# Kernel optimization log

Hardware: AMD Instinct MI355X
Metric: run time of the kernel (lower is better)

## Reference

```python
import jax, jax.numpy as jnp
import numpy as np

N_NODES = 100000
N_EDGES = 1600000
S_FEAT = 16   # static node features
D_FEAT = 8    # dynamic node features
E_FEAT = 4    # edge features
K = 2
EDGE_IN = E_FEAT + 2 * S_FEAT + 2 * D_FEAT  # 52
HIDDEN = 2 * D_FEAT                          # 16


def setup_inputs() -> dict:
    key = jax.random.key(0)
    ks = jax.random.split(key, 12)
    inp = {
        "x_s": jax.random.normal(ks[0], (N_NODES, S_FEAT), jnp.float32),
        "x_d": jax.random.normal(ks[1], (N_NODES, D_FEAT), jnp.float32),
        "edge_attr": jax.random.normal(ks[2], (N_EDGES, E_FEAT), jnp.float32),
        # edge MLP: Linear(EDGE_IN->HIDDEN) + ReLU + Linear(HIDDEN->D_FEAT)
        "W1": jax.random.normal(ks[3], (HIDDEN, EDGE_IN), jnp.float32) / np.sqrt(EDGE_IN),
        "b1": jnp.zeros((HIDDEN,), jnp.float32),
        "W2": jax.random.normal(ks[4], (D_FEAT, HIDDEN), jnp.float32) / np.sqrt(HIDDEN),
        "b2": jnp.zeros((D_FEAT,), jnp.float32),
        # K+1 = 3 filter matrices, Linear(D->D, bias=False): y = x @ W.T
        "Wf0": jax.random.normal(ks[5], (D_FEAT, D_FEAT), jnp.float32) / np.sqrt(D_FEAT),
        "Wf1": jax.random.normal(ks[6], (D_FEAT, D_FEAT), jnp.float32) / np.sqrt(D_FEAT),
        "Wf2": jax.random.normal(ks[7], (D_FEAT, D_FEAT), jnp.float32) / np.sqrt(D_FEAT),
        "edge_index": jax.random.randint(ks[8], (2, N_EDGES), 0, N_NODES, jnp.int64
                                         if jax.config.jax_enable_x64 else jnp.int32),
    }
    return inp


def _edge_mlp(e, W1, b1, W2, b2):
    h = jax.nn.relu(e @ W1.T + b1)
    return h @ W2.T + b2


def reference(x_s, x_d, edge_attr, W1, b1, W2, b2, Wf0, Wf1, Wf2, edge_index):
    row, col = edge_index[0], edge_index[1]
    num_nodes = x_d.shape[0]

    # s_ij depends only on static inputs (x_s, x_d, edge_attr), not on `out`,
    # so it is identical across the K steps; compute it once. The per-step
    # boolean edge mask is applied multiplicatively below, which matches the
    # torch masked-gather/scatter exactly (normalization is per-edge).
    e_ij = jnp.concatenate(
        [x_s[row], x_s[col], x_d[row], x_d[col], edge_attr], axis=1)  # [E, 52]
    s_ij = _edge_mlp(e_ij, W1, b1, W2, b2)                            # [E, D]
    nrm = jnp.linalg.norm(s_ij, axis=1, keepdims=True)
    s_ij = jnp.where(nrm > 0, s_ij / jnp.where(nrm > 0, nrm, 1.0), 0.0)

    filters = [Wf0, Wf1, Wf2]
    out = x_d @ filters[0].T
    for k in range(K):
        mask = out.sum(1) != 0                         # [N]
        edge_mask = (mask[row] | mask[col]).astype(out.dtype)  # [E]
        hydraulic_gradient = out[col] - out[row]       # [E, D]
        shift_sum = hydraulic_gradient * s_ij * edge_mask[:, None]
        scattered = jax.ops.segment_sum(shift_sum, col, num_segments=num_nodes)
        scattered = scattered @ filters[k + 1].T
        out = out + scattered
    return out
```

## Files before the change

kernel.cpp:

```cpp
#include <hip/hip_runtime.h>

#define S_FEAT 16
#define D_FEAT 8
#define E_FEAT 4
#define EDGE_IN 52
#define HIDDEN 16
#define SCAN_CHUNK 2048
#define NSUB 8

typedef unsigned int uint4v __attribute__((ext_vector_type(4)));

__device__ __forceinline__ void mlp_sij(
    const float* __restrict__ x_s, const float* __restrict__ x_d,
    const float* __restrict__ edge_attr,
    const float* __restrict__ W1, const float* __restrict__ b1,
    const float* __restrict__ W2, const float* __restrict__ b2,
    int row, int col, int e, float s[D_FEAT])
{
    float in[EDGE_IN];
    {
        const float4* p = (const float4*)(x_s + (size_t)row * S_FEAT);
#pragma unroll
        for (int q = 0; q < 4; ++q) {
            float4 v = p[q];
            in[q * 4 + 0] = v.x; in[q * 4 + 1] = v.y;
            in[q * 4 + 2] = v.z; in[q * 4 + 3] = v.w;
        }
    }
    {
        const float4* p = (const float4*)(x_s + (size_t)col * S_FEAT);
#pragma unroll
        for (int q = 0; q < 4; ++q) {
            float4 v = p[q];
            in[16 + q * 4 + 0] = v.x; in[16 + q * 4 + 1] = v.y;
            in[16 + q * 4 + 2] = v.z; in[16 + q * 4 + 3] = v.w;
        }
    }
    {
        const float4* p = (const float4*)(x_d + (size_t)row * D_FEAT);
#pragma unroll
        for (int q = 0; q < 2; ++q) {
            float4 v = p[q];
            in[32 + q * 4 + 0] = v.x; in[32 + q * 4 + 1] = v.y;
            in[32 + q * 4 + 2] = v.z; in[32 + q * 4 + 3] = v.w;
        }
    }
    {
        const float4* p = (const float4*)(x_d + (size_t)col * D_FEAT);
#pragma unroll
        for (int q = 0; q < 2; ++q) {
            float4 v = p[q];
            in[40 + q * 4 + 0] = v.x; in[40 + q * 4 + 1] = v.y;
            in[40 + q * 4 + 2] = v.z; in[40 + q * 4 + 3] = v.w;
        }
    }
    {
        float4 v = *(const float4*)(edge_attr + (size_t)e * E_FEAT);
        in[48] = v.x; in[49] = v.y; in[50] = v.z; in[51] = v.w;
    }

    float h[HIDDEN];
#pragma unroll
    for (int i = 0; i < HIDDEN; ++i) {
        float acc = b1[i];
#pragma unroll
        for (int j = 0; j < EDGE_IN; ++j)
            acc = fmaf(in[j], W1[i * EDGE_IN + j], acc);
        h[i] = acc > 0.f ? acc : 0.f;
    }

    float nrm2 = 0.f;
#pragma unroll
    for (int i = 0; i < D_FEAT; ++i) {
        float acc = b2[i];
#pragma unroll
        for (int j = 0; j < HIDDEN; ++j)
            acc = fmaf(h[j], W2[i * HIDDEN + j], acc);
        s[i] = acc;
        nrm2 = fmaf(acc, acc, nrm2);
    }
    float nrm = sqrtf(nrm2);
    float inv = nrm > 0.f ? 1.f / nrm : 0.f;
#pragma unroll
    for (int i = 0; i < D_FEAT; ++i) s[i] *= inv;
}

__device__ __forceinline__ uint4v pack_rec(const float s[8], int row)
{
    int q[8];
#pragma unroll
    for (int i = 0; i < 8; ++i) {
        float v = fminf(fmaxf(s[i] * 2047.f, -2047.f), 2047.f);
        q[i] = (int)rintf(v) & 0xFFF;
    }
    uint4v r;
    r[0] = (unsigned)(q[0] | (q[1] << 12) | (q[2] << 24));
    r[1] = (unsigned)((q[2] >> 8) | (q[3] << 4) | (q[4] << 16) | (q[5] << 28));
    r[2] = (unsigned)((q[5] >> 4) | (q[6] << 8) | (q[7] << 20));
    r[3] = (unsigned)row;
    return r;
}

__device__ __forceinline__ float rec_s(uint4v r, int f)
{
    int off = f * 12;
    unsigned lo = off < 32 ? r[0] : (off < 64 ? r[1] : r[2]);
    unsigned hi = off < 32 ? r[1] : (off < 64 ? r[2] : 0u);
    unsigned sh = (unsigned)off & 31u;
    unsigned long long both = ((unsigned long long)hi << 32) | lo;
    int q = ((int)((unsigned)(both >> sh) << 20)) >> 20;
    return (float)q * (1.f / 2047.f);
}

__global__ __launch_bounds__(256) void zero_counts_kernel(int* __restrict__ counts, int M)
{
    int i = blockIdx.x * blockDim.x + threadIdx.x;
    if (i < M) counts[i] = 0;
}

__global__ __launch_bounds__(256) void hist_kernel(
    const int* __restrict__ ei, int E, int N, int* __restrict__ counts8)
{
    int e = blockIdx.x * blockDim.x + threadIdx.x;
    if (e >= E) return;
    int col = ei[E + e];
    atomicAdd(&counts8[(threadIdx.x & (NSUB - 1)) * N + col], 1);
}

__global__ __launch_bounds__(256) void scan_local_kernel(
    const int* __restrict__ counts8, int* __restrict__ partial,
    int* __restrict__ blocksums, int N)
{
    __shared__ int sh[256];
    int b = blockIdx.x, t = threadIdx.x;
    int base = b * SCAN_CHUNK + t * 8;
    int v[8];
    int run = 0;
#pragma unroll
    for (int j = 0; j < 8; ++j) {
        int c = 0;
        if (base + j < N) {
#pragma unroll
            for (int s8 = 0; s8 < NSUB; ++s8)
                c += counts8[s8 * N + base + j];
        }
        v[j] = run;
        run += c;
    }
    sh[t] = run;
    __syncthreads();
#pragma unroll
    for (int st = 1; st < 256; st <<= 1) {
        int x = (t >= st) ? sh[t - st] : 0;
        __syncthreads();
        sh[t] += x;
        __syncthreads();
    }
    int excl = sh[t] - run;
    if (t == 255) blocksums[b] = sh[255];
#pragma unroll
    for (int j = 0; j < 8; ++j)
        if (base + j < N) partial[base + j] = excl + v[j];
}

__global__ void scan_blk_kernel(int* __restrict__ blocksums, int NB)
{
    if (threadIdx.x == 0) {
        int run = 0;
        for (int i = 0; i < NB; ++i) { int c = blocksums[i]; blocksums[i] = run; run += c; }
    }
}

__global__ __launch_bounds__(256) void scan_add_kernel(
    int* __restrict__ offsets, int* __restrict__ cursor,
    const int* __restrict__ blocksums, int N, int E)
{
    int i = blockIdx.x * blockDim.x + threadIdx.x;
    if (i < N) {
        int off = offsets[i] + blocksums[i / SCAN_CHUNK];
        offsets[i] = off;
        cursor[i]  = off;
    } else if (i == N) {
        offsets[N] = E;
    }
}

__global__ __launch_bounds__(256) void mlp_scatter_kernel(
    const float* __restrict__ x_s, const float* __restrict__ x_d,
    const float* __restrict__ edge_attr,
    const float* __restrict__ W1, const float* __restrict__ b1,
    const float* __restrict__ W2, const float* __restrict__ b2,
    const int* __restrict__ ei, int E,
    int* __restrict__ cursor, uint4v* __restrict__ recs)
{
    int e = blockIdx.x * blockDim.x + threadIdx.x;
    if (e >= E) return;
    int row = ei[e], col = ei[E + e];
    float s[D_FEAT];
    mlp_sij(x_s, x_d, edge_attr, W1, b1, W2, b2, row, col, e, s);
    uint4v rec = pack_rec(s, row);
    int pos = atomicAdd(&cursor[col], 1);
    __builtin_nontemporal_store(rec, recs + pos);
}

__global__ __launch_bounds__(256) void node_init_kernel(
    const float* __restrict__ x_d, const float* __restrict__ Wf0,
    float* __restrict__ out, unsigned char* __restrict__ mask, int N)
{
    int n = blockIdx.x * blockDim.x + threadIdx.x;
    if (n >= N) return;
    float xd[D_FEAT];
    {
        const float4* p = (const float4*)(x_d + (size_t)n * D_FEAT);
        float4 a = p[0], b = p[1];
        xd[0] = a.x; xd[1] = a.y; xd[2] = a.z; xd[3] = a.w;
        xd[4] = b.x; xd[5] = b.y; xd[6] = b.z; xd[7] = b.w;
    }
    float o[D_FEAT];
    float rs = 0.f;
#pragma unroll
    for (int i = 0; i < D_FEAT; ++i) {
        float acc = 0.f;
#pragma unroll
        for (int j = 0; j < D_FEAT; ++j)
            acc = fmaf(xd[j], Wf0[i * D_FEAT + j], acc);
        o[i] = acc;
        rs += acc;
    }
    float4* op = (float4*)(out + (size_t)n * D_FEAT);
    op[0] = make_float4(o[0], o[1], o[2], o[3]);
    op[1] = make_float4(o[4], o[5], o[6], o[7]);
    mask[n] = (rs != 0.f) ? 1 : 0;
}

__global__ __launch_bounds__(256) void csr_step_kernel(
    const float* __restrict__ out_in, float* __restrict__ out_out,
    const unsigned char* __restrict__ mask_in, unsigned char* __restrict__ mask_out,
    const int* __restrict__ offsets, const uint4v* __restrict__ recs,
    const float* __restrict__ Wf, int N)
{
    int lane = threadIdx.x & 63;
    int node = blockIdx.x * 4 + (threadIdx.x >> 6);
    if (node >= N) return;
    int e_sub = lane >> 3, f = lane & 7;
    int beg = offsets[node], end = offsets[node + 1];
    float outc = out_in[(size_t)node * 8 + f];
    int mc = mask_in[node];
    float acc = 0.f;
    for (int base = beg; base < end; base += 8) {
        int e = base + e_sub;
        bool valid = e < end;
        uint4v rec = (uint4v)(0u);
        if (valid) rec = __builtin_nontemporal_load(recs + e);
        int row = (int)rec[3];
        float s = rec_s(rec, f);
        float outr = out_in[(size_t)row * 8 + f];
        int m = mc | (int)mask_in[row];
        acc += (m != 0) ? (outc - outr) * s : 0.f;
    }
    acc += __shfl_xor(acc, 8);
    acc += __shfl_xor(acc, 16);
    acc += __shfl_xor(acc, 32);
    float upd = 0.f;
#pragma unroll
    for (int j = 0; j < 8; ++j) {
        float aj = __shfl(acc, (lane & ~7) | j);
        upd = fmaf(Wf[f * 8 + j], aj, upd);
    }
    float o = outc + upd;
    float rs = o;
    rs += __shfl_xor(rs, 1);
    rs += __shfl_xor(rs, 2);
    rs += __shfl_xor(rs, 4);
    if (e_sub == 0) {
        out_out[(size_t)node * 8 + f] = o;
        if (f == 0) mask_out[node] = (rs != 0.f) ? 1 : 0;
    }
}

__global__ __launch_bounds__(256) void fb_node_init_kernel(
    const float* __restrict__ x_d, const float* __restrict__ Wf0,
    float* __restrict__ out, float* __restrict__ scattered, int N)
{
    int n = blockIdx.x * blockDim.x + threadIdx.x;
    if (n >= N) return;
    float xd[D_FEAT];
    const float4* p = (const float4*)(x_d + (size_t)n * D_FEAT);
    float4 a = p[0], b = p[1];
    xd[0] = a.x; xd[1] = a.y; xd[2] = a.z; xd[3] = a.w;
    xd[4] = b.x; xd[5] = b.y; xd[6] = b.z; xd[7] = b.w;
    float o[D_FEAT];
#pragma unroll
    for (int i = 0; i < D_FEAT; ++i) {
        float acc = 0.f;
#pragma unroll
        for (int j = 0; j < D_FEAT; ++j)
            acc = fmaf(xd[j], Wf0[i * D_FEAT + j], acc);
        o[i] = acc;
    }
    float4* op = (float4*)(out + (size_t)n * D_FEAT);
    op[0] = make_float4(o[0], o[1], o[2], o[3]);
    op[1] = make_float4(o[4], o[5], o[6], o[7]);
    float4* sp = (float4*)(scattered + (size_t)n * D_FEAT);
    sp[0] = make_float4(0.f, 0.f, 0.f, 0.f);
    sp[1] = make_float4(0.f, 0.f, 0.f, 0.f);
}

__global__ __launch_bounds__(256) void fb_edge_step_kernel(
    const float* __restrict__ x_s, const float* __restrict__ x_d,
    const float* __restrict__ edge_attr,
    const float* __restrict__ W1, const float* __restrict__ b1,
    const float* __restrict__ W2, const float* __restrict__ b2,
    const float* __restrict__ out,
    const int* __restrict__ ei, int E, float* __restrict__ scattered)
{
    int e = blockIdx.x * blockDim.x + threadIdx.x;
    if (e >= E) return;
    int row = ei[e], col = ei[E + e];
    const float4* pr = (const float4*)(out + (size_t)row * D_FEAT);
    const float4* pc = (const float4*)(out + (size_t)col * D_FEAT);
    float4 r0 = pr[0], r1 = pr[1], c0 = pc[0], c1 = pc[1];
    float srow = r0.x + r0.y + r0.z + r0.w + r1.x + r1.y + r1.z + r1.w;
    float scol = c0.x + c0.y + c0.z + c0.w + c1.x + c1.y + c1.z + c1.w;
    if (srow == 0.f && scol == 0.f) return;
    float s[D_FEAT];
    mlp_sij(x_s, x_d, edge_attr, W1, b1, W2, b2, row, col, e, s);
    float* dst = scattered + (size_t)col * D_FEAT;
    atomicAdd(dst + 0, (c0.x - r0.x) * s[0]);
    atomicAdd(dst + 1, (c0.y - r0.y) * s[1]);
    atomicAdd(dst + 2, (c0.z - r0.z) * s[2]);
    atomicAdd(dst + 3, (c0.w - r0.w) * s[3]);
    atomicAdd(dst + 4, (c1.x - r1.x) * s[4]);
    atomicAdd(dst + 5, (c1.y - r1.y) * s[5]);
    atomicAdd(dst + 6, (c1.z - r1.z) * s[6]);
    atomicAdd(dst + 7, (c1.w - r1.w) * s[7]);
}

__global__ __launch_bounds__(256) void fb_node_update_kernel(
    float* __restrict__ out, float* __restrict__ scattered,
    const float* __restrict__ Wf, int N)
{
    int n = blockIdx.x * blockDim.x + threadIdx.x;
    if (n >= N) return;
    float sc[D_FEAT];
    float4* sp = (float4*)(scattered + (size_t)n * D_FEAT);
    float4 a = sp[0], b = sp[1];
    sc[0] = a.x; sc[1] = a.y; sc[2] = a.z; sc[3] = a.w;
    sc[4] = b.x; sc[5] = b.y; sc[6] = b.z; sc[7] = b.w;
    sp[0] = make_float4(0.f, 0.f, 0.f, 0.f);
    sp[1] = make_float4(0.f, 0.f, 0.f, 0.f);
    float4* op = (float4*)(out + (size_t)n * D_FEAT);
    float4 o0 = op[0], o1 = op[1];
    float o[D_FEAT] = {o0.x, o0.y, o0.z, o0.w, o1.x, o1.y, o1.z, o1.w};
#pragma unroll
    for (int i = 0; i < D_FEAT; ++i) {
        float acc = 0.f;
#pragma unroll
        for (int j = 0; j < D_FEAT; ++j)
            acc = fmaf(sc[j], Wf[i * D_FEAT + j], acc);
        o[i] += acc;
    }
    op[0] = make_float4(o[0], o[1], o[2], o[3]);
    op[1] = make_float4(o[4], o[5], o[6], o[7]);
}

extern "C" void kernel_launch(void* const* d_in, const int* in_sizes, int n_in,
                              void* d_out, int out_size, void* d_ws, size_t ws_size,
                              hipStream_t stream) {
    const float* x_s       = (const float*)d_in[0];
    const float* x_d       = (const float*)d_in[1];
    const float* edge_attr = (const float*)d_in[2];
    const float* W1        = (const float*)d_in[3];
    const float* b1        = (const float*)d_in[4];
    const float* W2        = (const float*)d_in[5];
    const float* b2        = (const float*)d_in[6];
    const float* Wf[3]     = {(const float*)d_in[7], (const float*)d_in[8],
                              (const float*)d_in[9]};
    const int*   ei        = (const int*)d_in[10];

    const int N = in_sizes[1] / D_FEAT;
    const int E = in_sizes[10] / 2;

    float* out = (float*)d_out;

    size_t off = 0;
    auto carve = [&](size_t bytes) { size_t p = off; off = (off + bytes + 255) & ~255ULL; return p; };
    size_t o_counts  = carve((size_t)NSUB * N * 4);
    size_t o_offsets = carve((size_t)(N + 1) * 4);
    size_t o_cursor  = carve((size_t)(N + 1) * 4);
    size_t o_bsums   = carve(256 * 4);
    size_t o_maskA   = carve((size_t)N);
    size_t o_maskB   = carve((size_t)N);
    size_t o_bufA    = carve((size_t)N * D_FEAT * 4);
    size_t o_recs    = carve((size_t)E * 16);
    const size_t need = off;

    dim3 blk(256);
    dim3 gE((E + 255) / 256);
    dim3 gN((N + 255) / 256);

    if (ws_size >= need) {
        char* ws = (char*)d_ws;
        int*   counts8 = (int*)(ws + o_counts);
        int*   offsets = (int*)(ws + o_offsets);
        int*   cursor  = (int*)(ws + o_cursor);
        int*   bsums   = (int*)(ws + o_bsums);
        unsigned char* maskA = (unsigned char*)(ws + o_maskA);
        unsigned char* maskB = (unsigned char*)(ws + o_maskB);
        float* bufA    = (float*)(ws + o_bufA);
        uint4v* recs   = (uint4v*)(ws + o_recs);

        const int NB = (N + SCAN_CHUNK - 1) / SCAN_CHUNK;

        zero_counts_kernel<<<dim3((NSUB * N + 255) / 256), blk, 0, stream>>>(counts8, NSUB * N);
        hist_kernel<<<gE, blk, 0, stream>>>(ei, E, N, counts8);
        scan_local_kernel<<<dim3(NB), blk, 0, stream>>>(counts8, offsets, bsums, N);
        scan_blk_kernel<<<dim3(1), dim3(64), 0, stream>>>(bsums, NB);
        scan_add_kernel<<<dim3((N + 256) / 256), blk, 0, stream>>>(offsets, cursor, bsums, N, E);

        node_init_kernel<<<gN, blk, 0, stream>>>(x_d, Wf[0], out, maskA, N);
        mlp_scatter_kernel<<<gE, blk, 0, stream>>>(
            x_s, x_d, edge_attr, W1, b1, W2, b2, ei, E, cursor, recs);

        dim3 gC((N + 3) / 4);
        csr_step_kernel<<<gC, blk, 0, stream>>>(
            out, bufA, maskA, maskB, offsets, recs, Wf[1], N);
        csr_step_kernel<<<gC, blk, 0, stream>>>(
            bufA, out, maskB, maskA, offsets, recs, Wf[2], N);
    } else {
        float* scattered = (float*)d_ws;
        fb_node_init_kernel<<<gN, blk, 0, stream>>>(x_d, Wf[0], out, scattered, N);
        for (int k = 0; k < 2; ++k) {
            fb_edge_step_kernel<<<gE, blk, 0, stream>>>(
                x_s, x_d, edge_attr, W1, b1, W2, b2, out, ei, E, scattered);
            fb_node_update_kernel<<<gN, blk, 0, stream>>>(out, scattered, Wf[k + 1], N);
        }
    }
}
```

Baseline: 419.7 us.

## Precompute per-node first-layer projections and derive masks from out in-register

Splits the first edge-MLP layer by linearity into per-node projections (row part with bias, col part) computed once per node. The edge kernel then gathers two 16-float vectors plus edge_attr instead of 48 input floats, and does only the 4-wide edge-feature part of the matmul. The per-node mask byte arrays are also removed: the CSR step recomputes each node's nonzero-sum mask from the gathered out row with lane shuffles. This trades extra workspace (two N×16 buffers) and one more launch, plus extra shuffles in the gather loop, for fewer FLOPs and a smaller per-edge gather.

```diff
diff --git a/kernel.cpp b/kernel.cpp
--- a/kernel.cpp
+++ b/kernel.cpp
@@ -185,7 +185,114 @@
     }
 }
 
-__global__ __launch_bounds__(256) void mlp_scatter_kernel(
+__global__ __launch_bounds__(256) void proj_kernel(
+    const float* __restrict__ x_s, const float* __restrict__ x_d,
+    const float* __restrict__ W1, const float* __restrict__ b1,
+    float* __restrict__ PR, float* __restrict__ PC, int N)
+{
+    int n = blockIdx.x * blockDim.x + threadIdx.x;
+    if (n >= N) return;
+    float xs[S_FEAT], xd[D_FEAT];
+    {
+        const float4* p = (const float4*)(x_s + (size_t)n * S_FEAT);
+#pragma unroll
+        for (int q = 0; q < 4; ++q) {
+            float4 v = p[q];
+            xs[q * 4 + 0] = v.x; xs[q * 4 + 1] = v.y;
+            xs[q * 4 + 2] = v.z; xs[q * 4 + 3] = v.w;
+        }
+        const float4* pd = (const float4*)(x_d + (size_t)n * D_FEAT);
+        float4 a = pd[0], b = pd[1];
+        xd[0] = a.x; xd[1] = a.y; xd[2] = a.z; xd[3] = a.w;
+        xd[4] = b.x; xd[5] = b.y; xd[6] = b.z; xd[7] = b.w;
+    }
+    float pr[HIDDEN], pc[HIDDEN];
+#pragma unroll
+    for (int i = 0; i < HIDDEN; ++i) {
+        const float* w = W1 + i * EDGE_IN;
+        float a = b1[i], c = 0.f;
+#pragma unroll
+        for (int j = 0; j < S_FEAT; ++j) {
+            a = fmaf(xs[j], w[j], a);
+            c = fmaf(xs[j], w[16 + j], c);
+        }
+#pragma unroll
+        for (int j = 0; j < D_FEAT; ++j) {
+            a = fmaf(xd[j], w[32 + j], a);
+            c = fmaf(xd[j], w[40 + j], c);
+        }
+        pr[i] = a; pc[i] = c;
+    }
+    float4* prp = (float4*)(PR + (size_t)n * HIDDEN);
+    float4* pcp = (float4*)(PC + (size_t)n * HIDDEN);
+#pragma unroll
+    for (int q = 0; q < 4; ++q) {
+        prp[q] = make_float4(pr[q * 4], pr[q * 4 + 1], pr[q * 4 + 2], pr[q * 4 + 3]);
+        pcp[q] = make_float4(pc[q * 4], pc[q * 4 + 1], pc[q * 4 + 2], pc[q * 4 + 3]);
+    }
+}
+
+__global__ __launch_bounds__(256) void mlp_scatter_proj_kernel(
+    const float* __restrict__ PR, const float* __restrict__ PC,
+    const float* __restrict__ edge_attr,
+    const float* __restrict__ W1,
+    const float* __restrict__ W2, const float* __restrict__ b2,
+    const int* __restrict__ ei, int E,
+    int* __restrict__ cursor, uint4v* __restrict__ recs)
+{
+    int e = blockIdx.x * blockDim.x + threadIdx.x;
+    if (e >= E) return;
+    int row = ei[e], col = ei[E + e];
+
+    float pr[HIDDEN], pc[HIDDEN];
+    {
+        const float4* p = (const float4*)(PR + (size_t)row * HIDDEN);
+        const float4* c = (const float4*)(PC + (size_t)col * HIDDEN);
+#pragma unroll
+        for (int q = 0; q < 4; ++q) {
+            float4 a = p[q], b = c[q];
+            pr[q * 4 + 0] = a.x; pr[q * 4 + 1] = a.y;
+            pr[q * 4 + 2] = a.z; pr[q * 4 + 3] = a.w;
+            pc[q * 4 + 0] = b.x; pc[q * 4 + 1] = b.y;
+            pc[q * 4 + 2] = b.z; pc[q * 4 + 3] = b.w;
+        }
+    }
+    float4 ea = *(const float4*)(edge_attr + (size_t)e * E_FEAT);
+
+    float h[HIDDEN];
+#pragma unroll
+    for (int i = 0; i < HIDDEN; ++i) {
+        const float* w = W1 + i * EDGE_IN + 48;
+        float acc = pr[i] + pc[i];
+        acc = fmaf(ea.x, w[0], acc);
+        acc = fmaf(ea.y, w[1], acc);
+        acc = fmaf(ea.z, w[2], acc);
+        acc = fmaf(ea.w, w[3], acc);
+        h[i] = acc > 0.f ? acc : 0.f;
+    }
+
+    float s[D_FEAT];
+    float nrm2 = 0.f;
+#pragma unroll
+    for (int i = 0; i < D_FEAT; ++i) {
+        float acc = b2[i];
+#pragma unroll
+        for (int j = 0; j < HIDDEN; ++j)
+            acc = fmaf(h[j], W2[i * HIDDEN + j], acc);
+        s[i] = acc;
+        nrm2 = fmaf(acc, acc, nrm2);
+    }
+    float nrm = sqrtf(nrm2);
+    float inv = nrm > 0.f ? 1.f / nrm : 0.f;
+#pragma unroll
+    for (int i = 0; i < D_FEAT; ++i) s[i] *= inv;
+
+    uint4v rec = pack_rec(s, row);
+    int pos = atomicAdd(&cursor[col], 1);
+    __builtin_nontemporal_store(rec, recs + pos);
+}
+
+__global__ __launch_bounds__(256) void mlp_scatter_direct_kernel(
     const float* __restrict__ x_s, const float* __restrict__ x_d,
     const float* __restrict__ edge_attr,
     const float* __restrict__ W1, const float* __restrict__ b1,
@@ -205,7 +312,7 @@
 
 __global__ __launch_bounds__(256) void node_init_kernel(
     const float* __restrict__ x_d, const float* __restrict__ Wf0,
-    float* __restrict__ out, unsigned char* __restrict__ mask, int N)
+    float* __restrict__ out, int N)
 {
     int n = blockIdx.x * blockDim.x + threadIdx.x;
     if (n >= N) return;
@@ -217,7 +324,6 @@
         xd[4] = b.x; xd[5] = b.y; xd[6] = b.z; xd[7] = b.w;
     }
     float o[D_FEAT];
-    float rs = 0.f;
 #pragma unroll
     for (int i = 0; i < D_FEAT; ++i) {
         float acc = 0.f;
@@ -225,17 +331,14 @@
         for (int j = 0; j < D_FEAT; ++j)
             acc = fmaf(xd[j], Wf0[i * D_FEAT + j], acc);
         o[i] = acc;
-        rs += acc;
     }
     float4* op = (float4*)(out + (size_t)n * D_FEAT);
     op[0] = make_float4(o[0], o[1], o[2], o[3]);
     op[1] = make_float4(o[4], o[5], o[6], o[7]);
-    mask[n] = (rs != 0.f) ? 1 : 0;
 }
 
 __global__ __launch_bounds__(256) void csr_step_kernel(
     const float* __restrict__ out_in, float* __restrict__ out_out,
-    const unsigned char* __restrict__ mask_in, unsigned char* __restrict__ mask_out,
     const int* __restrict__ offsets, const uint4v* __restrict__ recs,
     const float* __restrict__ Wf, int N)
 {
@@ -245,7 +348,9 @@
     int e_sub = lane >> 3, f = lane & 7;
     int beg = offsets[node], end = offsets[node + 1];
     float outc = out_in[(size_t)node * 8 + f];
-    int mc = mask_in[node];
+    float sc = outc;
+    sc += __shfl_xor(sc, 1); sc += __shfl_xor(sc, 2); sc += __shfl_xor(sc, 4);
+    bool mc = (sc != 0.f);
     float acc = 0.f;
     for (int base = beg; base < end; base += 8) {
         int e = base + e_sub;
@@ -255,8 +360,10 @@
         int row = (int)rec[3];
         float s = rec_s(rec, f);
         float outr = out_in[(size_t)row * 8 + f];
-        int m = mc | (int)mask_in[row];
-        acc += (m != 0) ? (outc - outr) * s : 0.f;
+        float sr = outr;
+        sr += __shfl_xor(sr, 1); sr += __shfl_xor(sr, 2); sr += __shfl_xor(sr, 4);
+        bool m = mc || (sr != 0.f);
+        acc += m ? (outc - outr) * s : 0.f;
     }
     acc += __shfl_xor(acc, 8);
     acc += __shfl_xor(acc, 16);
@@ -267,15 +374,8 @@
         float aj = __shfl(acc, (lane & ~7) | j);
         upd = fmaf(Wf[f * 8 + j], aj, upd);
     }
-    float o = outc + upd;
-    float rs = o;
-    rs += __shfl_xor(rs, 1);
-    rs += __shfl_xor(rs, 2);
-    rs += __shfl_xor(rs, 4);
-    if (e_sub == 0) {
-        out_out[(size_t)node * 8 + f] = o;
-        if (f == 0) mask_out[node] = (rs != 0.f) ? 1 : 0;
-    }
+    if (e_sub == 0)
+        out_out[(size_t)node * 8 + f] = outc + upd;
 }
 
 __global__ __launch_bounds__(256) void fb_node_init_kernel(
@@ -389,24 +489,23 @@
     size_t o_offsets = carve((size_t)(N + 1) * 4);
     size_t o_cursor  = carve((size_t)(N + 1) * 4);
     size_t o_bsums   = carve(256 * 4);
-    size_t o_maskA   = carve((size_t)N);
-    size_t o_maskB   = carve((size_t)N);
     size_t o_bufA    = carve((size_t)N * D_FEAT * 4);
     size_t o_recs    = carve((size_t)E * 16);
-    const size_t need = off;
+    const size_t need_base = off;
+    size_t o_PR      = carve((size_t)N * HIDDEN * 4);
+    size_t o_PC      = carve((size_t)N * HIDDEN * 4);
+    const size_t need_full = off;
 
     dim3 blk(256);
     dim3 gE((E + 255) / 256);
     dim3 gN((N + 255) / 256);
 
-    if (ws_size >= need) {
+    if (ws_size >= need_base) {
         char* ws = (char*)d_ws;
         int*   counts8 = (int*)(ws + o_counts);
         int*   offsets = (int*)(ws + o_offsets);
         int*   cursor  = (int*)(ws + o_cursor);
         int*   bsums   = (int*)(ws + o_bsums);
-        unsigned char* maskA = (unsigned char*)(ws + o_maskA);
-        unsigned char* maskB = (unsigned char*)(ws + o_maskB);
         float* bufA    = (float*)(ws + o_bufA);
         uint4v* recs   = (uint4v*)(ws + o_recs);
 
@@ -418,15 +517,22 @@
         scan_blk_kernel<<<dim3(1), dim3(64), 0, stream>>>(bsums, NB);
         scan_add_kernel<<<dim3((N + 256) / 256), blk, 0, stream>>>(offsets, cursor, bsums, N, E);
 
-        node_init_kernel<<<gN, blk, 0, stream>>>(x_d, Wf[0], out, maskA, N);
-        mlp_scatter_kernel<<<gE, blk, 0, stream>>>(
-            x_s, x_d, edge_attr, W1, b1, W2, b2, ei, E, cursor, recs);
+        node_init_kernel<<<gN, blk, 0, stream>>>(x_d, Wf[0], out, N);
+
+        if (ws_size >= need_full) {
+            float* PR = (float*)(ws + o_PR);
+            float* PC = (float*)(ws + o_PC);
+            proj_kernel<<<gN, blk, 0, stream>>>(x_s, x_d, W1, b1, PR, PC, N);
+            mlp_scatter_proj_kernel<<<gE, blk, 0, stream>>>(
+                PR, PC, edge_attr, W1, W2, b2, ei, E, cursor, recs);
+        } else {
+            mlp_scatter_direct_kernel<<<gE, blk, 0, stream>>>(
+                x_s, x_d, edge_attr, W1, b1, W2, b2, ei, E, cursor, recs);
+        }
 
         dim3 gC((N + 3) / 4);
-        csr_step_kernel<<<gC, blk, 0, stream>>>(
-            out, bufA, maskA, maskB, offsets, recs, Wf[1], N);
-        csr_step_kernel<<<gC, blk, 0, stream>>>(
-            bufA, out, maskB, maskA, offsets, recs, Wf[2], N);
+        csr_step_kernel<<<gC, blk, 0, stream>>>(out, bufA, offsets, recs, Wf[1], N);
+        csr_step_kernel<<<gC, blk, 0, stream>>>(bufA, out, offsets, recs, Wf[2], N);
     } else {
         float* scattered = (float*)d_ws;
         fb_node_init_kernel<<<gN, blk, 0, stream>>>(x_d, Wf[0], out, scattered, N);
```

Result: faster. 386.5 us (-7.9%).
